# Performance work log

Hardware: AMD Instinct MI355X
Metric: run time of the kernel (lower is better)

Reference implementation:

```python
import jax, jax.numpy as jnp
import numpy as np

THRESHOLD = 0.1
NORM_EPS = 1e-12
DEG_EPS = 1e-6


def setup_inputs() -> dict:
    key = jax.random.key(0)
    k1, k2, k3, k4 = jax.random.split(key, 4)
    N, D_STATE, F_IN, F_OUT = 8192, 16, 256, 256
    node_features = jax.random.normal(k1, (N, F_IN), dtype=jnp.float32)
    states = jax.random.normal(k2, (N, D_STATE), dtype=jnp.float32)
    W = jax.random.normal(k3, (F_OUT, F_IN), dtype=jnp.float32) * (1.0 / np.sqrt(F_IN))
    b = jax.random.normal(k4, (F_OUT,), dtype=jnp.float32) * 0.01
    return {"node_features": node_features, "states": states, "W": W, "b": b}


def reference(node_features, states, W, b):
    # Pairwise fidelity: fid[i,j] = (<s_i/|s_i|, s_j/|s_j|>)^2
    s = states / (jnp.linalg.norm(states, axis=1, keepdims=True) + NORM_EPS)
    fid = jnp.square(s @ s.T)  # [N, N]
    N = fid.shape[0]
    # Edge if fid >= threshold; graph has no self-loops (combinations skips i==j)
    adj = jnp.where(fid >= THRESHOLD, 1.0, 0.0).astype(node_features.dtype)
    adj = adj * (1.0 - jnp.eye(N, dtype=node_features.dtype))
    # deg = diag(1/(rowsum+eps)); agg = (adj @ deg) @ X  == column-scaled adj @ X
    deg_inv = 1.0 / (adj.sum(axis=1) + DEG_EPS)  # [N]
    agg = (adj * deg_inv[None, :]) @ node_features  # [N, F_in]
    return agg @ W.T + b
```

## Files before the change

### kernel.cpp

```cpp
#include <hip/hip_runtime.h>
#include <hip/hip_bf16.h>

typedef __attribute__((ext_vector_type(8))) short short8;
typedef __attribute__((ext_vector_type(4))) float f32x4;
typedef __attribute__((ext_vector_type(4))) unsigned int u32x4;
typedef unsigned short u16;
typedef unsigned int   u32;
typedef unsigned long long u64;
typedef unsigned char  u8;

#define NN 8192
#define THRESH 0.1f

__device__ __forceinline__ u16 f2bf(float f){
  __hip_bfloat16 h = __float2bfloat16(f);
  u16 u; __builtin_memcpy(&u, &h, 2); return u;
}
__device__ __forceinline__ float bf2f(u16 h){
  u32 u = ((u32)h) << 16;
  return __builtin_bit_cast(float, u);
}

__global__ __launch_bounds__(256) void k_norm(const float* __restrict__ st, u16* __restrict__ snT){
  int i = blockIdx.x*256 + threadIdx.x;
  const float4* s4 = reinterpret_cast<const float4*>(st + i*16);
  float4 v[4]; float ss = 0.f;
  #pragma unroll
  for (int q=0;q<4;q++){ v[q]=s4[q]; ss += v[q].x*v[q].x+v[q].y*v[q].y+v[q].z*v[q].z+v[q].w*v[q].w; }
  float inv = 1.0f/(sqrtf(ss) + 1e-12f);
  float f[16];
  #pragma unroll
  for (int q=0;q<4;q++){ f[4*q]=v[q].x*inv; f[4*q+1]=v[q].y*inv; f[4*q+2]=v[q].z*inv; f[4*q+3]=v[q].w*inv; }
  u16 hb[16], lb[16];
  #pragma unroll
  for (int k=0;k<16;k++){
    u16 h = f2bf(f[k]);
    hb[k] = h;
    lb[k] = f2bf(f[k] - bf2f(h));
  }
  u16* dst = snT + (size_t)(i >> 4)*512 + (i & 15)*8;
  short8 o;
  #pragma unroll
  for (int e=0;e<8;e++) o[e] = (short)hb[e];
  *reinterpret_cast<short8*>(dst)       = o;
  #pragma unroll
  for (int e=0;e<8;e++) o[e] = (short)hb[8+e];
  *reinterpret_cast<short8*>(dst + 128) = o;
  #pragma unroll
  for (int e=0;e<8;e++) o[e] = (short)lb[e];
  *reinterpret_cast<short8*>(dst + 256) = o;
  #pragma unroll
  for (int e=0;e<8;e++) o[e] = (short)lb[8+e];
  *reinterpret_cast<short8*>(dst + 384) = o;
}

__global__ __launch_bounds__(256, 6) void k_maskM2(const u16* __restrict__ snT, u32* __restrict__ maskT){
  int tid = threadIdx.x;
  int lane = tid & 63, wid = tid >> 6;
  int n = lane & 15, g = lane >> 4;
  int bid = (int)blockIdx.x;
  int i0w = (bid >> 4) * 128 + wid * 32;
  int jc = (bid & 15) * 512;

  short8 b1[2], b2[2];
  #pragma unroll
  for (int p=0; p<2; ++p){
    const u16* bblk = snT + (size_t)((i0w >> 4) + p)*512;
    b1[p] = *reinterpret_cast<const short8*>(bblk + (g&1)*128 + n*8);
    b2[p] = *reinterpret_cast<const short8*>(bblk + (2+(g&1))*128 + n*8);
  }

  u32 bitc[2][4];
  #pragma unroll
  for (int h=0; h<2; ++h)
    #pragma unroll
    for (int q=0; q<4; ++q) bitc[h][q] = 1u << (h*16 + 4*g + q);

  #pragma unroll 2
  for (int jw2 = 0; jw2 < 16; ++jw2){
    int j0 = jc + jw2*32;
    u32 w0 = 0, w1 = 0;
    #pragma unroll
    for (int h=0; h<2; ++h){
      short8 a = *reinterpret_cast<const short8*>(snT + (size_t)((j0 >> 4) + h)*512 + lane*8);
      f32x4 acc0 = {0.f,0.f,0.f,0.f};
      f32x4 acc1 = {0.f,0.f,0.f,0.f};
      acc0 = __builtin_amdgcn_mfma_f32_16x16x32_bf16(a, b2[0], acc0, 0, 0, 0);
      acc1 = __builtin_amdgcn_mfma_f32_16x16x32_bf16(a, b2[1], acc1, 0, 0, 0);
      acc0 = __builtin_amdgcn_mfma_f32_16x16x32_bf16(a, b1[0], acc0, 0, 0, 0);
      acc1 = __builtin_amdgcn_mfma_f32_16x16x32_bf16(a, b1[1], acc1, 0, 0, 0);
      #pragma unroll
      for (int q=0;q<4;q++){
        float d0 = acc0[q], d1 = acc1[q];
        w0 |= (d0*d0 >= THRESH) ? bitc[h][q] : 0u;
        w1 |= (d1*d1 >= THRESH) ? bitc[h][q] : 0u;
      }
    }
    w0 |= __shfl_xor(w0, 16);
    w0 |= __shfl_xor(w0, 32);
    w1 |= __shfl_xor(w1, 16);
    w1 |= __shfl_xor(w1, 32);
    int jw = j0 >> 5;
    int ii0 = i0w + n, ii1 = i0w + 16 + n;
    if ((ii0 >> 5) == jw) w0 &= ~(1u << (ii0 & 31));
    if ((ii1 >> 5) == jw) w1 &= ~(1u << (ii1 & 31));
    if (lane < 16){
      maskT[(size_t)jw*NN + ii0] = w0;
      maskT[(size_t)jw*NN + ii1] = w1;
    }
  }
}

__global__ __launch_bounds__(256) void k_deg(const u32* __restrict__ maskT, float* __restrict__ dinvF){
  __shared__ u32 red[256];
  int tid = threadIdx.x;
  int il = tid & 31, ws = tid >> 5;
  int i = blockIdx.x*32 + il;
  u32 s = 0;
  #pragma unroll 8
  for (int w = ws*32; w < ws*32 + 32; ++w) s += __popc(maskT[(size_t)w*NN + i]);
  red[tid] = s;
  __syncthreads();
  if (tid < 32){
    u32 tot = 0;
    #pragma unroll
    for (int g=0; g<8; ++g) tot += red[g*32 + tid];
    dinvF[i] = 1.0f/((float)tot + 1e-6f);
  }
}

__global__ __launch_bounds__(128) void k_ygemm(const float* __restrict__ X, const float* __restrict__ W,
                                               const float* __restrict__ dinvF, u16* __restrict__ Yt){
  int tid = threadIdx.x;
  int lane = tid & 63;
  int r = lane & 15, g = lane >> 4;
  int wj = tid >> 6;
  int f0 = blockIdx.x * 32;
  int j0 = blockIdx.y * 128 + wj * 64;
  f32x4 acc[2][4] = {};
  #pragma unroll
  for (int k0 = 0; k0 < 256; k0 += 32){
    short8 a[2], b[4];
    #pragma unroll
    for (int af=0; af<2; af++){
      const float* p = W + (f0 + af*16 + r)*256 + k0 + g*8;
      float4 u = reinterpret_cast<const float4*>(p)[0];
      float4 v = reinterpret_cast<const float4*>(p)[1];
      short8 tt;
      tt[0]=(short)f2bf(u.x); tt[1]=(short)f2bf(u.y); tt[2]=(short)f2bf(u.z); tt[3]=(short)f2bf(u.w);
      tt[4]=(short)f2bf(v.x); tt[5]=(short)f2bf(v.y); tt[6]=(short)f2bf(v.z); tt[7]=(short)f2bf(v.w);
      a[af] = tt;
    }
    #pragma unroll
    for (int bf=0; bf<4; bf++){
      const float* p = X + (j0 + bf*16 + r)*256 + k0 + g*8;
      float4 u = reinterpret_cast<const float4*>(p)[0];
      float4 v = reinterpret_cast<const float4*>(p)[1];
      short8 tt;
      tt[0]=(short)f2bf(u.x); tt[1]=(short)f2bf(u.y); tt[2]=(short)f2bf(u.z); tt[3]=(short)f2bf(u.w);
      tt[4]=(short)f2bf(v.x); tt[5]=(short)f2bf(v.y); tt[6]=(short)f2bf(v.z); tt[7]=(short)f2bf(v.w);
      b[bf] = tt;
    }
    #pragma unroll
    for (int af=0; af<2; af++)
      #pragma unroll
      for (int bf=0; bf<4; bf++)
        acc[af][bf] = __builtin_amdgcn_mfma_f32_16x16x32_bf16(a[af], b[bf], acc[af][bf], 0, 0, 0);
  }
  float ds[4];
  #pragma unroll
  for (int bf=0;bf<4;bf++) ds[bf] = dinvF[j0 + bf*16 + r];
  #pragma unroll
  for (int af=0; af<2; af++)
    #pragma unroll
    for (int bf=0; bf<4; bf++)
      #pragma unroll
      for (int q=0;q<4;q++)
        Yt[(f0 + af*16 + g*4 + q)*NN + j0 + bf*16 + r] = f2bf(acc[af][bf][q] * ds[bf]);
}

#define VMCNT(N) asm volatile("s_waitcnt vmcnt(" #N ")" ::: "memory")
__global__ __launch_bounds__(512, 4) void k_agg(const u16* __restrict__ Yt, const u32* __restrict__ maskT,
                                                u16* __restrict__ part){
  __shared__ u8  ldsB[3][16384];
  __shared__ u32 ldsM[3][512];
  int tid = threadIdx.x;
  int lane = tid & 63, wid = tid >> 6;
  int r = lane & 15, g = lane >> 4;
  int wm = wid >> 1, wn = wid & 1;
  int bid = (int)blockIdx.x;
  int gq = bid & 15;
  int m0 = (bid >> 4) * 256;
  int n0 = (gq & 1) * 128;
  int zz = gq >> 1;
  int kbase = zz * 1024;
  f32x4 acc[4][4] = {};

  const char* ytb[2];
  #pragma unroll
  for (int is=0; is<2; ++is){
    int rw = wid*16 + is*8 + (lane>>3);
    ytb[is] = (const char*)(Yt + ((size_t)(n0+rw) << 13) + (size_t)kbase + (size_t)(((lane&7) ^ (rw&7))<<3));
  }
  const char* mkb = (const char*)(maskT + (size_t)((kbase>>5) + (lane&1))*NN + m0 + wid*32 + (lane>>1));

#define GSTAGE(BUF, T) do { \
    _Pragma("unroll") \
    for (int is=0; is<2; ++is) \
      __builtin_amdgcn_global_load_lds((const __attribute__((address_space(1))) void*)(ytb[is] + (T)*128), \
          (__attribute__((address_space(3))) void*)&ldsB[BUF][wid*2048 + is*1024], 16, 0, 0); \
    __builtin_amdgcn_global_load_lds((const __attribute__((address_space(1))) void*)(mkb + (size_t)(T)*65536), \
        (__attribute__((address_space(3))) void*)&ldsM[BUF][wid*64], 4, 0, 0); \
  } while(0)

#define COMPUTE(BUF) do { \
    short8 bfrag[2][4]; \
    _Pragma("unroll") \
    for (int kk=0; kk<2; ++kk) \
      _Pragma("unroll") \
      for (int nf=0; nf<4; ++nf){ \
        int row = wn*64 + nf*16 + r; \
        bfrag[kk][nf] = *reinterpret_cast<const short8*>(&ldsB[BUF][row*128 + (((kk*4+g) ^ (row&7))<<4)]); \
      } \
    __builtin_amdgcn_s_setprio(1); \
    _Pragma("unroll") \
    for (int mf=0; mf<4; ++mf){ \
      int rowm = wm*64 + mf*16 + r; \
      u64 mw = *reinterpret_cast<const u64*>(&ldsM[BUF][rowm*2]); \
      _Pragma("unroll") \
      for (int kk=0; kk<2; ++kk){ \
        u32 byte = ((u32)(mw >> (kk*32)) >> (g*8)) & 0xffu; \
        u32 x = byte * 0x8001u; \
        u32x4 wv; \
        _Pragma("unroll") \
        for (int pp=0; pp<4; ++pp) wv[pp] = ((x >> (2*pp)) & 0x00010001u) * 0x3F80u; \
        short8 a = __builtin_bit_cast(short8, wv); \
        _Pragma("unroll") \
        for (int nf=0; nf<4; ++nf) \
          acc[mf][nf] = __builtin_amdgcn_mfma_f32_16x16x32_bf16(a, bfrag[kk][nf], acc[mf][nf], 0, 0, 0); \
      } \
    } \
    __builtin_amdgcn_s_setprio(0); \
  } while(0)

#define BODY(CB, SB, T) do { \
    GSTAGE(SB, (T)+2); \
    COMPUTE(CB); \
    VMCNT(3); \
    __builtin_amdgcn_s_barrier(); \
  } while(0)

  GSTAGE(0, 0);
  GSTAGE(1, 1);
  VMCNT(3);
  __builtin_amdgcn_s_barrier();

  #pragma unroll 1
  for (int t = 0; t < 12; t += 3){
    BODY(0, 2, t);
    BODY(1, 0, t+1);
    BODY(2, 1, t+2);
  }
  BODY(0, 2, 12);
  BODY(1, 0, 13);
  COMPUTE(2);
  VMCNT(0);
  __builtin_amdgcn_s_barrier();
  COMPUTE(0);

#undef GSTAGE
#undef COMPUTE
#undef BODY

  u16* dst = part + (size_t)zz * (NN*256);
  #pragma unroll
  for (int mf=0; mf<4; mf++)
    #pragma unroll
    for (int nf=0; nf<4; nf++)
      #pragma unroll
      for (int q=0;q<4;q++){
        int row = m0 + wm*64 + mf*16 + g*4 + q;
        int col = n0 + wn*64 + nf*16 + r;
        dst[row*256 + col] = f2bf(acc[mf][nf][q]);
      }
}

__global__ __launch_bounds__(256) void k_reduce(const u16* __restrict__ part, const float* __restrict__ bias,
                                                float* __restrict__ out){
  int i = blockIdx.x*256 + threadIdx.x;
  float4 bb = reinterpret_cast<const float4*>(bias)[i & 63];
  float a0 = bb.x, a1 = bb.y, a2 = bb.z, a3 = bb.w;
  #pragma unroll
  for (int z=0; z<8; ++z){
    u64 v = *reinterpret_cast<const u64*>(part + (size_t)z*2097152 + (size_t)i*4);
    a0 += bf2f((u16)(v      ));
    a1 += bf2f((u16)(v >> 16));
    a2 += bf2f((u16)(v >> 32));
    a3 += bf2f((u16)(v >> 48));
  }
  float4 o; o.x=a0; o.y=a1; o.z=a2; o.w=a3;
  reinterpret_cast<float4*>(out)[i] = o;
}

extern "C" void kernel_launch(void* const* d_in, const int* in_sizes, int n_in,
                              void* d_out, int out_size, void* d_ws, size_t ws_size,
                              hipStream_t stream) {
  const float* X    = (const float*)d_in[0];
  const float* S    = (const float*)d_in[1];
  const float* W    = (const float*)d_in[2];
  const float* bias = (const float*)d_in[3];
  float* out = (float*)d_out;
  char* ws = (char*)d_ws;
  u32*   maskT = (u32*)  (ws + 0);
  u16*   Yt    = (u16*)  (ws + 8388608);
  u16*   snT   = (u16*)  (ws + 12582912);
  float* dinvF = (float*)(ws + 13107200);
  u16*   part  = (u16*)  (ws + 13139968);

  k_norm  <<<dim3(32),   dim3(256), 0, stream>>>(S, snT);
  k_maskM2<<<dim3(1024), dim3(256), 0, stream>>>(snT, maskT);
  k_deg   <<<dim3(256),  dim3(256), 0, stream>>>(maskT, dinvF);
  k_ygemm <<<dim3(8,64), dim3(128), 0, stream>>>(X, W, dinvF, Yt);
  k_agg   <<<dim3(512),  dim3(512), 0, stream>>>(Yt, maskT, part);
  k_reduce<<<dim3(2048), dim3(256), 0, stream>>>(part, bias, out);
}
```

Baseline: 85.63 us.

## Drop LDS staging in aggregation kernel; load operands directly into registers

The aggregation GEMM no longer stages Yt tiles and mask words through triple-buffered LDS with barriers. Each of the 4 waves now owns a 64-column strip over 128 rows and loads B fragments and mask words straight from global memory into registers, using double-buffered register fragments. This removes LDS traffic and block-wide barriers, but loses data sharing across waves, so global/L2 load traffic grows and register pressure rises with the 8x4 accumulators.

```diff
diff --git a/kernel.cpp b/kernel.cpp
--- a/kernel.cpp
+++ b/kernel.cpp
@@ -179,57 +179,41 @@
         Yt[(f0 + af*16 + g*4 + q)*NN + j0 + bf*16 + r] = f2bf(acc[af][bf][q] * ds[bf]);
 }
 
-#define VMCNT(N) asm volatile("s_waitcnt vmcnt(" #N ")" ::: "memory")
-__global__ __launch_bounds__(512, 4) void k_agg(const u16* __restrict__ Yt, const u32* __restrict__ maskT,
+__global__ __launch_bounds__(256, 2) void k_agg(const u16* __restrict__ Yt, const u32* __restrict__ maskT,
                                                 u16* __restrict__ part){
-  __shared__ u8  ldsB[3][16384];
-  __shared__ u32 ldsM[3][512];
   int tid = threadIdx.x;
   int lane = tid & 63, wid = tid >> 6;
   int r = lane & 15, g = lane >> 4;
-  int wm = wid >> 1, wn = wid & 1;
   int bid = (int)blockIdx.x;
-  int gq = bid & 15;
-  int m0 = (bid >> 4) * 256;
-  int n0 = (gq & 1) * 128;
-  int zz = gq >> 1;
+  int zz = bid & 7;
+  int m0 = (bid >> 3) * 128;
+  int n0 = wid * 64;
   int kbase = zz * 1024;
-  f32x4 acc[4][4] = {};
-
-  const char* ytb[2];
-  #pragma unroll
-  for (int is=0; is<2; ++is){
-    int rw = wid*16 + is*8 + (lane>>3);
-    ytb[is] = (const char*)(Yt + ((size_t)(n0+rw) << 13) + (size_t)kbase + (size_t)(((lane&7) ^ (rw&7))<<3));
-  }
-  const char* mkb = (const char*)(maskT + (size_t)((kbase>>5) + (lane&1))*NN + m0 + wid*32 + (lane>>1));
-
-#define GSTAGE(BUF, T) do { \
+  f32x4 acc[8][4] = {};
+
+  const u16* yb = Yt + (size_t)(n0 + r)*NN + (size_t)kbase + g*8;
+  const u32* mb = maskT + (size_t)(kbase >> 5)*NN + m0 + r;
+
+#define LOADBF(T, BF) do { \
     _Pragma("unroll") \
-    for (int is=0; is<2; ++is) \
-      __builtin_amdgcn_global_load_lds((const __attribute__((address_space(1))) void*)(ytb[is] + (T)*128), \
-          (__attribute__((address_space(3))) void*)&ldsB[BUF][wid*2048 + is*1024], 16, 0, 0); \
-    __builtin_amdgcn_global_load_lds((const __attribute__((address_space(1))) void*)(mkb + (size_t)(T)*65536), \
-        (__attribute__((address_space(3))) void*)&ldsM[BUF][wid*64], 4, 0, 0); \
+    for (int nf=0; nf<4; ++nf) \
+      _Pragma("unroll") \
+      for (int kk=0; kk<2; ++kk) \
+        BF[kk][nf] = *reinterpret_cast<const short8*>(yb + (size_t)nf*16*NN + (T)*64 + kk*32); \
   } while(0)
 
-#define COMPUTE(BUF) do { \
-    short8 bfrag[2][4]; \
+#define COMPUTE(T, BF) do { \
+    u32 mk[2][8]; \
     _Pragma("unroll") \
-    for (int kk=0; kk<2; ++kk) \
+    for (int mf=0; mf<8; ++mf) \
       _Pragma("unroll") \
-      for (int nf=0; nf<4; ++nf){ \
-        int row = wn*64 + nf*16 + r; \
-        bfrag[kk][nf] = *reinterpret_cast<const short8*>(&ldsB[BUF][row*128 + (((kk*4+g) ^ (row&7))<<4)]); \
-      } \
-    __builtin_amdgcn_s_setprio(1); \
+      for (int kk=0; kk<2; ++kk) \
+        mk[kk][mf] = mb[(size_t)(2*(T)+kk)*NN + mf*16]; \
     _Pragma("unroll") \
-    for (int mf=0; mf<4; ++mf){ \
-      int rowm = wm*64 + mf*16 + r; \
-      u64 mw = *reinterpret_cast<const u64*>(&ldsM[BUF][rowm*2]); \
+    for (int mf=0; mf<8; ++mf){ \
       _Pragma("unroll") \
       for (int kk=0; kk<2; ++kk){ \
-        u32 byte = ((u32)(mw >> (kk*32)) >> (g*8)) & 0xffu; \
+        u32 byte = (mk[kk][mf] >> (g*8)) & 0xffu; \
         u32 x = byte * 0x8001u; \
         u32x4 wv; \
         _Pragma("unroll") \
@@ -237,50 +221,33 @@
         short8 a = __builtin_bit_cast(short8, wv); \
         _Pragma("unroll") \
         for (int nf=0; nf<4; ++nf) \
-          acc[mf][nf] = __builtin_amdgcn_mfma_f32_16x16x32_bf16(a, bfrag[kk][nf], acc[mf][nf], 0, 0, 0); \
+          acc[mf][nf] = __builtin_amdgcn_mfma_f32_16x16x32_bf16(a, BF[kk][nf], acc[mf][nf], 0, 0, 0); \
       } \
     } \
-    __builtin_amdgcn_s_setprio(0); \
   } while(0)
 
-#define BODY(CB, SB, T) do { \
-    GSTAGE(SB, (T)+2); \
-    COMPUTE(CB); \
-    VMCNT(3); \
-    __builtin_amdgcn_s_barrier(); \
-  } while(0)
-
-  GSTAGE(0, 0);
-  GSTAGE(1, 1);
-  VMCNT(3);
-  __builtin_amdgcn_s_barrier();
-
+  short8 bfA[2][4], bfB[2][4];
+  LOADBF(0, bfA);
   #pragma unroll 1
-  for (int t = 0; t < 12; t += 3){
-    BODY(0, 2, t);
-    BODY(1, 0, t+1);
-    BODY(2, 1, t+2);
-  }
-  BODY(0, 2, 12);
-  BODY(1, 0, 13);
-  COMPUTE(2);
-  VMCNT(0);
-  __builtin_amdgcn_s_barrier();
-  COMPUTE(0);
-
-#undef GSTAGE
+  for (int t = 0; t < 16; t += 2){
+    LOADBF(t+1, bfB);
+    COMPUTE(t, bfA);
+    if (t + 2 < 16) LOADBF(t+2, bfA);
+    COMPUTE(t+1, bfB);
+  }
+
+#undef LOADBF
 #undef COMPUTE
-#undef BODY
 
   u16* dst = part + (size_t)zz * (NN*256);
   #pragma unroll
-  for (int mf=0; mf<4; mf++)
+  for (int mf=0; mf<8; mf++)
     #pragma unroll
     for (int nf=0; nf<4; nf++)
       #pragma unroll
       for (int q=0;q<4;q++){
-        int row = m0 + wm*64 + mf*16 + g*4 + q;
-        int col = n0 + wn*64 + nf*16 + r;
+        int row = m0 + mf*16 + g*4 + q;
+        int col = n0 + nf*16 + r;
         dst[row*256 + col] = f2bf(acc[mf][nf][q]);
       }
 }
@@ -321,6 +288,6 @@
   k_maskM2<<<dim3(1024), dim3(256), 0, stream>>>(snT, maskT);
   k_deg   <<<dim3(256),  dim3(256), 0, stream>>>(maskT, dinvF);
   k_ygemm <<<dim3(8,64), dim3(128), 0, stream>>>(X, W, dinvF, Yt);
-  k_agg   <<<dim3(512),  dim3(512), 0, stream>>>(Yt, maskT, part);
+  k_agg   <<<dim3(512),  dim3(256), 0, stream>>>(Yt, maskT, part);
   k_reduce<<<dim3(2048), dim3(256), 0, stream>>>(part, bias, out);
 }
```

Measured after the change: 97.29 us. 1.14x slower.

## Fuse state normalization and degree counting into mask kernel

Applied to the files above, without the earlier changes.

Normalization of the state vectors now runs inside the mask kernel: each block computes the split bf16 hi/lo values for its i and j rows and stages them in LDS, replacing the separate k_norm launch and its global buffer. Row degrees are accumulated from per-lane popcounts with atomicAdd into a counter array that is zeroed by a memset, which removes the k_deg pass that re-read the whole mask. k_ygemm now computes the inverse degree from the counts. The cost is redundant normalization work in every block, extra LDS use that may lower occupancy, and an added memset plus atomics.

```diff
diff --git a/kernel.cpp b/kernel.cpp
--- a/kernel.cpp
+++ b/kernel.cpp
@@ -21,51 +21,61 @@
   return __builtin_bit_cast(float, u);
 }
 
-__global__ __launch_bounds__(256) void k_norm(const float* __restrict__ st, u16* __restrict__ snT){
-  int i = blockIdx.x*256 + threadIdx.x;
-  const float4* s4 = reinterpret_cast<const float4*>(st + i*16);
-  float4 v[4]; float ss = 0.f;
-  #pragma unroll
-  for (int q=0;q<4;q++){ v[q]=s4[q]; ss += v[q].x*v[q].x+v[q].y*v[q].y+v[q].z*v[q].z+v[q].w*v[q].w; }
-  float inv = 1.0f/(sqrtf(ss) + 1e-12f);
-  float f[16];
-  #pragma unroll
-  for (int q=0;q<4;q++){ f[4*q]=v[q].x*inv; f[4*q+1]=v[q].y*inv; f[4*q+2]=v[q].z*inv; f[4*q+3]=v[q].w*inv; }
-  u16 hb[16], lb[16];
-  #pragma unroll
-  for (int k=0;k<16;k++){
-    u16 h = f2bf(f[k]);
-    hb[k] = h;
-    lb[k] = f2bf(f[k] - bf2f(h));
-  }
-  u16* dst = snT + (size_t)(i >> 4)*512 + (i & 15)*8;
-  short8 o;
-  #pragma unroll
-  for (int e=0;e<8;e++) o[e] = (short)hb[e];
-  *reinterpret_cast<short8*>(dst)       = o;
-  #pragma unroll
-  for (int e=0;e<8;e++) o[e] = (short)hb[8+e];
-  *reinterpret_cast<short8*>(dst + 128) = o;
-  #pragma unroll
-  for (int e=0;e<8;e++) o[e] = (short)lb[e];
-  *reinterpret_cast<short8*>(dst + 256) = o;
-  #pragma unroll
-  for (int e=0;e<8;e++) o[e] = (short)lb[8+e];
-  *reinterpret_cast<short8*>(dst + 384) = o;
-}
-
-__global__ __launch_bounds__(256, 6) void k_maskM2(const u16* __restrict__ snT, u32* __restrict__ maskT){
+__global__ __launch_bounds__(256) void k_maskM2F(const float* __restrict__ st, u32* __restrict__ maskT,
+                                                 u32* __restrict__ degcnt){
+  __shared__ __align__(16) u16 ldsJ[32*512];
+  __shared__ __align__(16) u16 ldsI[8*512];
   int tid = threadIdx.x;
   int lane = tid & 63, wid = tid >> 6;
   int n = lane & 15, g = lane >> 4;
   int bid = (int)blockIdx.x;
-  int i0w = (bid >> 4) * 128 + wid * 32;
-  int jc = (bid & 15) * 512;
+  int i0b = (bid >> 4) * 128;
+  int jc  = (bid & 15) * 512;
+  int i0w = i0b + wid * 32;
+
+#define NORMROW(ROW, DST) do { \
+    const float4* s4_ = reinterpret_cast<const float4*>(st + (size_t)(ROW)*16); \
+    float4 v_[4]; float ss_ = 0.f; \
+    _Pragma("unroll") \
+    for (int q=0;q<4;q++){ v_[q]=s4_[q]; ss_ += v_[q].x*v_[q].x+v_[q].y*v_[q].y+v_[q].z*v_[q].z+v_[q].w*v_[q].w; } \
+    float inv_ = 1.0f/(sqrtf(ss_) + 1e-12f); \
+    float f_[16]; \
+    _Pragma("unroll") \
+    for (int q=0;q<4;q++){ f_[4*q]=v_[q].x*inv_; f_[4*q+1]=v_[q].y*inv_; f_[4*q+2]=v_[q].z*inv_; f_[4*q+3]=v_[q].w*inv_; } \
+    u16 hb_[16], lb_[16]; \
+    _Pragma("unroll") \
+    for (int k=0;k<16;k++){ u16 h_ = f2bf(f_[k]); hb_[k] = h_; lb_[k] = f2bf(f_[k] - bf2f(h_)); } \
+    u16* d_ = (DST); \
+    short8 o_; \
+    _Pragma("unroll") \
+    for (int e=0;e<8;e++) o_[e] = (short)hb_[e]; \
+    *reinterpret_cast<short8*>(d_)       = o_; \
+    _Pragma("unroll") \
+    for (int e=0;e<8;e++) o_[e] = (short)hb_[8+e]; \
+    *reinterpret_cast<short8*>(d_ + 128) = o_; \
+    _Pragma("unroll") \
+    for (int e=0;e<8;e++) o_[e] = (short)lb_[e]; \
+    *reinterpret_cast<short8*>(d_ + 256) = o_; \
+    _Pragma("unroll") \
+    for (int e=0;e<8;e++) o_[e] = (short)lb_[8+e]; \
+    *reinterpret_cast<short8*>(d_ + 384) = o_; \
+  } while(0)
+
+  {
+    int lj0 = tid;
+    int lj1 = tid + 256;
+    NORMROW(jc + lj0, ldsJ + (lj0 >> 4)*512 + (lj0 & 15)*8);
+    NORMROW(jc + lj1, ldsJ + (lj1 >> 4)*512 + (lj1 & 15)*8);
+    if (tid < 128)
+      NORMROW(i0b + tid, ldsI + (tid >> 4)*512 + (tid & 15)*8);
+  }
+#undef NORMROW
+  __syncthreads();
 
   short8 b1[2], b2[2];
   #pragma unroll
   for (int p=0; p<2; ++p){
-    const u16* bblk = snT + (size_t)((i0w >> 4) + p)*512;
+    const u16* bblk = ldsI + (wid*2 + p)*512;
     b1[p] = *reinterpret_cast<const short8*>(bblk + (g&1)*128 + n*8);
     b2[p] = *reinterpret_cast<const short8*>(bblk + (2+(g&1))*128 + n*8);
   }
@@ -75,6 +85,9 @@
   for (int h=0; h<2; ++h)
     #pragma unroll
     for (int q=0; q<4; ++q) bitc[h][q] = 1u << (h*16 + 4*g + q);
+
+  int ii0 = i0w + n, ii1 = i0w + 16 + n;
+  u32 pc0 = 0, pc1 = 0;
 
   #pragma unroll 2
   for (int jw2 = 0; jw2 < 16; ++jw2){
@@ -82,7 +95,7 @@
     u32 w0 = 0, w1 = 0;
     #pragma unroll
     for (int h=0; h<2; ++h){
-      short8 a = *reinterpret_cast<const short8*>(snT + (size_t)((j0 >> 4) + h)*512 + lane*8);
+      short8 a = *reinterpret_cast<const short8*>(ldsJ + (jw2*2 + h)*512 + lane*8);
       f32x4 acc0 = {0.f,0.f,0.f,0.f};
       f32x4 acc1 = {0.f,0.f,0.f,0.f};
       acc0 = __builtin_amdgcn_mfma_f32_16x16x32_bf16(a, b2[0], acc0, 0, 0, 0);
@@ -101,36 +114,23 @@
     w1 |= __shfl_xor(w1, 16);
     w1 |= __shfl_xor(w1, 32);
     int jw = j0 >> 5;
-    int ii0 = i0w + n, ii1 = i0w + 16 + n;
     if ((ii0 >> 5) == jw) w0 &= ~(1u << (ii0 & 31));
     if ((ii1 >> 5) == jw) w1 &= ~(1u << (ii1 & 31));
     if (lane < 16){
       maskT[(size_t)jw*NN + ii0] = w0;
       maskT[(size_t)jw*NN + ii1] = w1;
+      pc0 += __popc(w0);
+      pc1 += __popc(w1);
     }
   }
-}
-
-__global__ __launch_bounds__(256) void k_deg(const u32* __restrict__ maskT, float* __restrict__ dinvF){
-  __shared__ u32 red[256];
-  int tid = threadIdx.x;
-  int il = tid & 31, ws = tid >> 5;
-  int i = blockIdx.x*32 + il;
-  u32 s = 0;
-  #pragma unroll 8
-  for (int w = ws*32; w < ws*32 + 32; ++w) s += __popc(maskT[(size_t)w*NN + i]);
-  red[tid] = s;
-  __syncthreads();
-  if (tid < 32){
-    u32 tot = 0;
-    #pragma unroll
-    for (int g=0; g<8; ++g) tot += red[g*32 + tid];
-    dinvF[i] = 1.0f/((float)tot + 1e-6f);
+  if (lane < 16){
+    atomicAdd(&degcnt[ii0], pc0);
+    atomicAdd(&degcnt[ii1], pc1);
   }
 }
 
 __global__ __launch_bounds__(128) void k_ygemm(const float* __restrict__ X, const float* __restrict__ W,
-                                               const float* __restrict__ dinvF, u16* __restrict__ Yt){
+                                               const u32* __restrict__ degcnt, u16* __restrict__ Yt){
   int tid = threadIdx.x;
   int lane = tid & 63;
   int r = lane & 15, g = lane >> 4;
@@ -169,7 +169,10 @@
   }
   float ds[4];
   #pragma unroll
-  for (int bf=0;bf<4;bf++) ds[bf] = dinvF[j0 + bf*16 + r];
+  for (int bf=0;bf<4;bf++){
+    u32 dg = degcnt[j0 + bf*16 + r];
+    ds[bf] = 1.0f/((float)dg + 1e-6f);
+  }
   #pragma unroll
   for (int af=0; af<2; af++)
     #pragma unroll
@@ -311,16 +314,14 @@
   const float* bias = (const float*)d_in[3];
   float* out = (float*)d_out;
   char* ws = (char*)d_ws;
-  u32*   maskT = (u32*)  (ws + 0);
-  u16*   Yt    = (u16*)  (ws + 8388608);
-  u16*   snT   = (u16*)  (ws + 12582912);
-  float* dinvF = (float*)(ws + 13107200);
-  u16*   part  = (u16*)  (ws + 13139968);
-
-  k_norm  <<<dim3(32),   dim3(256), 0, stream>>>(S, snT);
-  k_maskM2<<<dim3(1024), dim3(256), 0, stream>>>(snT, maskT);
-  k_deg   <<<dim3(256),  dim3(256), 0, stream>>>(maskT, dinvF);
-  k_ygemm <<<dim3(8,64), dim3(128), 0, stream>>>(X, W, dinvF, Yt);
-  k_agg   <<<dim3(512),  dim3(512), 0, stream>>>(Yt, maskT, part);
-  k_reduce<<<dim3(2048), dim3(256), 0, stream>>>(part, bias, out);
-}
+  u32*   maskT  = (u32*)(ws + 0);
+  u16*   Yt     = (u16*)(ws + 8388608);
+  u32*   degcnt = (u32*)(ws + 12582912);
+  u16*   part   = (u16*)(ws + 13139968);
+
+  hipMemsetAsync(degcnt, 0, 8192*sizeof(u32), stream);
+  k_maskM2F<<<dim3(1024), dim3(256), 0, stream>>>(S, maskT, degcnt);
+  k_ygemm  <<<dim3(8,64), dim3(128), 0, stream>>>(X, W, degcnt, Yt);
+  k_agg    <<<dim3(512),  dim3(512), 0, stream>>>(Yt, maskT, part);
+  k_reduce <<<dim3(2048), dim3(256), 0, stream>>>(part, bias, out);
+}
```

Result: no change. 86.37 us (+0.9%).
